# Kernel tuning notes

Measured on AMD Instinct MI355X. Metric: run time of the kernel, lower is better.

Reference implementation:

```python
import jax, jax.numpy as jnp
import numpy as np

N_HEAD, D_HEAD, D_MODEL = 16, 64, 1024
QLEN, MEMLEN, BSZ = 1024, 1024, 2
KLEN = QLEN + MEMLEN  # rlen == klen
LN_EPS = 1e-5
NEG = -1e30


def _rel_shift(x):
    # x: [qlen, rlen, bsz, n_head] -> Transformer-XL relative shift
    q, r, b, n = x.shape
    zp = jnp.zeros((q, 1, b, n), x.dtype)
    xp = jnp.concatenate([zp, x], axis=1).reshape(r + 1, q, b, n)
    return xp[1:].reshape(q, r, b, n)


def _layer_norm(x, gamma, beta):
    mu = jnp.mean(x, axis=-1, keepdims=True)
    var = jnp.mean((x - mu) ** 2, axis=-1, keepdims=True)
    return (x - mu) * jax.lax.rsqrt(var + LN_EPS) * gamma + beta


def setup_inputs() -> dict:
    key = jax.random.key(0)
    ks = jax.random.split(key, 8)
    w = jax.random.normal(ks[0], (QLEN, BSZ, D_MODEL), jnp.float32)
    r = jax.random.normal(ks[1], (KLEN, D_MODEL), jnp.float32)
    r_w_bias = jax.random.normal(ks[2], (N_HEAD, D_HEAD), jnp.float32) * 0.02
    r_r_bias = jax.random.normal(ks[3], (N_HEAD, D_HEAD), jnp.float32) * 0.02
    mems = jax.random.normal(ks[4], (MEMLEN, BSZ, D_MODEL), jnp.float32)
    W_qkv = jax.random.normal(ks[5], (D_MODEL, 3 * N_HEAD * D_HEAD), jnp.float32) * 0.02
    W_r = jax.random.normal(ks[6], (D_MODEL, N_HEAD * D_HEAD), jnp.float32) * 0.02
    W_o = jax.random.normal(ks[7], (N_HEAD * D_HEAD, D_MODEL), jnp.float32) * 0.02
    ln_gamma = jnp.ones((D_MODEL,), jnp.float32)
    ln_beta = jnp.zeros((D_MODEL,), jnp.float32)
    # causal mask with memory: key j visible to query i iff j <= i + MEMLEN (True = keep)
    attn_mask = jnp.arange(KLEN)[None, :] <= (jnp.arange(QLEN)[:, None] + MEMLEN)
    return {"w": w, "r": r, "r_w_bias": r_w_bias, "r_r_bias": r_r_bias,
            "mems": mems, "attn_mask": attn_mask, "W_qkv": W_qkv, "W_r": W_r,
            "W_o": W_o, "ln_gamma": ln_gamma, "ln_beta": ln_beta}


def reference(w, r, r_w_bias, r_r_bias, mems, attn_mask, W_qkv, W_r, W_o, ln_gamma, ln_beta):
    qlen, bsz = w.shape[0], w.shape[1]
    scale = 1.0 / (D_HEAD ** 0.5)
    cat = jnp.concatenate([mems, w], axis=0)            # [klen, b, d_model]
    klen = cat.shape[0]
    w_heads = cat @ W_qkv                                # [klen, b, 3*H*D]
    r_head_k = (r @ W_r).reshape(-1, N_HEAD, D_HEAD)     # [rlen, H, D]
    w_head_q, w_head_k, w_head_v = jnp.split(w_heads, 3, axis=-1)
    w_head_q = w_head_q[-qlen:].reshape(qlen, bsz, N_HEAD, D_HEAD)
    w_head_k = w_head_k.reshape(klen, bsz, N_HEAD, D_HEAD)
    w_head_v = w_head_v.reshape(klen, bsz, N_HEAD, D_HEAD)
    AC = jnp.einsum('ibnd,jbnd->ijbn', w_head_q + r_w_bias, w_head_k)
    BD = jnp.einsum('ibnd,jnd->ijbn', w_head_q + r_r_bias, r_head_k)
    BD = _rel_shift(BD)
    attn_score = (AC + BD) * scale                       # [q, k, b, n]
    attn_score = jnp.where(attn_mask[:, :, None, None], attn_score, NEG)
    attn_prob = jax.nn.softmax(attn_score, axis=1)
    attn_vec = jnp.einsum('ijbn,jbnd->ibnd', attn_prob, w_head_v)
    attn_vec = attn_vec.reshape(qlen, bsz, N_HEAD * D_HEAD)
    attn_out = attn_vec @ W_o                            # [q, b, d_model]
    return _layer_norm(w + attn_out, ln_gamma, ln_beta)
```

## Files before the change

kernel.cpp:

```cpp
#include <hip/hip_runtime.h>
#include <hip/hip_bf16.h>

#define NHEAD 16
#define DHEAD 64
#define DMODEL 1024
#define QLEN 1024
#define MEMLEN 1024
#define BSZ 2
#define KLEN 2048
#define LN_EPS 1e-5f

typedef __hip_bfloat16 bf16;
typedef __attribute__((ext_vector_type(8))) short short8;
typedef __attribute__((ext_vector_type(4))) float f32x4;

__device__ __forceinline__ float b2f(bf16 x) { return __bfloat162float(x); }
__device__ __forceinline__ bf16 f2b(float x) { return __float2bfloat16(x); }
__device__ __forceinline__ short f2bs(float f) {
    bf16 h = __float2bfloat16(f);
    return *reinterpret_cast<short*>(&h);
}
__device__ __forceinline__ float s2f(short s) {
    bf16 h = *reinterpret_cast<bf16*>(&s);
    return __bfloat162float(h);
}
__device__ __forceinline__ float fexp2(float x) {
    float y;
    asm("v_exp_f32 %0, %1" : "=v"(y) : "v"(x));
    return y;
}

#define MFMA16(a, b, c) __builtin_amdgcn_mfma_f32_16x16x32_bf16(a, b, c, 0, 0, 0)

#define AS1 __attribute__((address_space(1)))
#define AS3 __attribute__((address_space(3)))
__device__ __forceinline__ void gld16(const bf16* g, bf16* l) {
    __builtin_amdgcn_global_load_lds((const AS1 void*)(uintptr_t)g,
                                     (AS3 void*)(uint32_t)(uintptr_t)l, 16, 0, 0);
}

__global__ __launch_bounds__(256)
void prep(const float* __restrict__ mems, const float* __restrict__ w,
          const float* __restrict__ r, const float* __restrict__ Wqkv,
          const float* __restrict__ Wr, const float* __restrict__ Wo,
          bf16* __restrict__ Abf, bf16* __restrict__ rbf,
          bf16* __restrict__ Wqkvt, bf16* __restrict__ Wrt,
          bf16* __restrict__ Wot) {
    __shared__ bf16 T[64][65];
    const int id = blockIdx.x;
    const int t = threadIdx.x;
    if (id < 6144) {
        const float* src;
        bf16* dst;
        int off;
        if (id < 2048)      { src = mems; dst = Abf;                       off = id; }
        else if (id < 4096) { src = w;    dst = Abf + (size_t)2048 * 1024; off = id - 2048; }
        else                { src = r;    dst = rbf;                       off = id - 4096; }
        int i = off * 256 + t;
        const float4 v = reinterpret_cast<const float4*>(src)[i];
        bf16 o[4] = {f2b(v.x), f2b(v.y), f2b(v.z), f2b(v.w)};
        reinterpret_cast<ulong1*>(dst)[i] = *reinterpret_cast<ulong1*>(o);
        return;
    }
    int tid2 = id - 6144;
    const float* in;
    bf16* out;
    int N, tn, tile;
    if (tid2 < 768)       { in = Wqkv; out = Wqkvt; N = 3072; tn = 48; tile = tid2; }
    else if (tid2 < 1024) { in = Wr;   out = Wrt;   N = 1024; tn = 16; tile = tid2 - 768; }
    else                  { in = Wo;   out = Wot;   N = 1024; tn = 16; tile = tid2 - 1024; }
    const int K = 1024;
    const int n0 = (tile % tn) * 64, k0 = (tile / tn) * 64;
    #pragma unroll
    for (int e = 0; e < 16; e++) {
        int flat = e * 256 + t;
        int kl = flat >> 6, nl = flat & 63;
        T[kl][nl] = f2b(in[(size_t)(k0 + kl) * N + n0 + nl]);
    }
    __syncthreads();
    #pragma unroll
    for (int e = 0; e < 16; e++) {
        int flat = e * 256 + t;
        int nl = flat >> 6, kl = flat & 63;
        out[(size_t)(n0 + nl) * K + k0 + kl] = T[kl][nl];
    }
}

__global__ __launch_bounds__(256)
void gemm_mfma(const bf16* __restrict__ A, const bf16* __restrict__ Bt,
               const bf16* __restrict__ A2, const bf16* __restrict__ B2,
               int M, int N, int K, int mode,
               const float* __restrict__ rwb, const float* __restrict__ rrb,
               bf16* __restrict__ Qw, bf16* __restrict__ Qr,
               bf16* __restrict__ Kb, bf16* __restrict__ Vt,
               bf16* __restrict__ Cb, float* __restrict__ Cf,
               float* __restrict__ Cf2) {
    const int bm = blockIdx.x * 128, bn = blockIdx.y * 128;
    int sub = 0;
    const bf16* Ap = A;
    const bf16* Bp = Bt;
    if (mode == 0 && bm < 2048 && bn < 1024) { sub = 1; Ap = A2; Bp = B2; }
    const int ldk = (mode == 2) ? 1024 : K;
    float* Cfz = Cf;
    if (mode == 2 && blockIdx.z) { Ap += 512; Bp += 512; Cfz = Cf2; }
    __shared__ bf16 As[2][128 * 32];
    __shared__ bf16 Bs[2][128 * 32];
    const int t = threadIdx.x;
    const int w = t >> 6, lane = t & 63, quad = lane >> 4, l16 = lane & 15;
    const int wm = (w >> 1) * 64, wn = (w & 1) * 64;
    const int lrow = lane >> 2, lcol = (lane & 3) * 8;

    auto stage = [&](int k0, int buf) {
        #pragma unroll
        for (int e = 0; e < 2; e++) {
            int ch = w + 4 * e;
            int row = ch * 16 + lrow;
            gld16(Ap + (size_t)(bm + row) * ldk + k0 + lcol, As[buf] + ch * 512);
            gld16(Bp + (size_t)(bn + row) * ldk + k0 + lcol, Bs[buf] + ch * 512);
        }
    };

    f32x4 acc[4][4];
    #pragma unroll
    for (int mt = 0; mt < 4; mt++)
        #pragma unroll
        for (int nt = 0; nt < 4; nt++) acc[mt][nt] = (f32x4){0.f, 0.f, 0.f, 0.f};

    stage(0, 0);
    const int NK = K >> 5;
    for (int kk = 0; kk < NK; kk++) {
        asm volatile("s_waitcnt vmcnt(0)" ::: "memory");
        __builtin_amdgcn_s_barrier();
        if (kk + 1 < NK) stage((kk + 1) << 5, (kk + 1) & 1);
        const bf16* A_ = As[kk & 1];
        const bf16* B_ = Bs[kk & 1];
        short8 af[4], bfr[4];
        #pragma unroll
        for (int mt = 0; mt < 4; mt++)
            af[mt] = *reinterpret_cast<const short8*>(&A_[(wm + 16 * mt + l16) * 32 + quad * 8]);
        #pragma unroll
        for (int nt = 0; nt < 4; nt++)
            bfr[nt] = *reinterpret_cast<const short8*>(&B_[(wn + 16 * nt + l16) * 32 + quad * 8]);
        #pragma unroll
        for (int mt = 0; mt < 4; mt++)
            #pragma unroll
            for (int nt = 0; nt < 4; nt++)
                acc[mt][nt] = MFMA16(af[mt], bfr[nt], acc[mt][nt]);
    }

    const float QSC = 0.18033688f;
    #pragma unroll
    for (int mt = 0; mt < 4; mt++)
        #pragma unroll
        for (int nt = 0; nt < 4; nt++)
            #pragma unroll
            for (int r = 0; r < 4; r++) {
                int m = bm + wm + 16 * mt + quad * 4 + r;
                int c = bn + wn + 16 * nt + l16;
                float v = acc[mt][nt][r];
                if (sub) {
                    Cb[(size_t)m * 1024 + c] = f2b(v);
                } else if (mode == 0) {
                    int seg = c >> 10, cc2 = c & 1023;
                    if (seg == 0) {
                        if (m >= 2048) {
                            size_t o = (size_t)(m - 2048) * 1024 + cc2;
                            Qw[o] = f2b((v + rwb[cc2]) * QSC);
                            Qr[o] = f2b((v + rrb[cc2]) * QSC);
                        }
                    } else if (seg == 1) {
                        Kb[(size_t)m * 1024 + cc2] = f2b(v);
                    } else {
                        int j = m >> 1, bb = m & 1;
                        int vn = cc2 >> 6, dd = cc2 & 63;
                        int ds = dd >> 4, l16v = dd & 15;
                        int jt = j >> 6, jl = j & 63;
                        int h = jl >> 5, qd = (jl >> 3) & 3, e = jl & 7;
                        size_t addr = ((size_t)(vn * 2 + bb) * 32 + jt) * 4096
                                    + (ds * 2 + h) * 512 + (qd * 16 + l16v) * 8 + e;
                        Vt[addr] = f2b(v);
                    }
                } else {
                    Cfz[(size_t)m * N + c] = v;
                }
            }
}

__global__ __launch_bounds__(256, 3)
void attn_mfma(const bf16* __restrict__ Qw, const bf16* __restrict__ Qr,
               const bf16* __restrict__ Kb, const bf16* __restrict__ Vt,
               const bf16* __restrict__ Rk, float* __restrict__ O0g,
               float* __restrict__ O1g, float2* __restrict__ ML) {
    const int id = blockIdx.x;
    const int xcd = id & 7, local = id >> 3;
    const int pidx = local & 3;
    const int couple = (local >> 2) & 7;
    const int chunk = local >> 5;
    const int pair = xcd * 4 + pidx;
    const int b = pair & 1, n = pair >> 1;
    const int TA = couple + 17;
    const int t_beg = (chunk == 0) ? 0 : (chunk == 1) ? 17 : 33;
    const int t_end = (chunk == 0) ? 17 : (chunk == 1) ? 33 : 49;

    int segs[2][4];
    int nseg = 0;
    {
        int aend = min(t_end, TA);
        if (t_beg < aend) {
            segs[nseg][0] = couple; segs[nseg][1] = t_beg;
            segs[nseg][2] = aend;   segs[nseg][3] = (t_beg == 0) ? 0 : 1;
            nseg++;
        }
        int bbeg = max(t_beg, TA);
        if (bbeg < t_end) {
            segs[nseg][0] = 15 - couple; segs[nseg][1] = bbeg - TA;
            segs[nseg][2] = t_end - TA;  segs[nseg][3] = (bbeg == TA) ? 0 : 1;
            nseg++;
        }
    }

    const int tid = threadIdx.x;
    const int w = tid >> 6, lane = tid & 63;
    const int quad = lane >> 4, l16 = lane & 15;
    const int ln8 = lane >> 3;
    const int cs = (lane & 7) ^ (ln8 & 7);
    const int q0 = (quad ^ (l16 & 7)) * 8;
    const int q1 = q0 ^ 32;
    const int rbl = 48 - 16 * w;

    __shared__ bf16 Ks[64 * 64];
    __shared__ bf16 Vs[64 * 64];
    __shared__ bf16 Rs[3][64 * 64];
    __shared__ short WP_s[4][16 * 82];
    short* WP = WP_s[w];

    const int koff = b * 1024 + n * 64 + cs * 8;
    const bf16* Vbase = Vt + (size_t)(n * 2 + b) * 131072 + lane * 8;
    const int rcol = n * 64 + cs * 8;

    for (int sg = 0; sg < nseg; sg++) {
        const int i0 = segs[sg][0], jb = segs[sg][1], je = segs[sg][2], slot = segs[sg][3];
        const int I0 = i0 * 64;
        const int qbase = I0 + 16 * w;
        const int RB = 960 - I0;
        const int jlast = i0 + 16;

        auto stageKV = [&](int tt) {
            const int J0t = tt * 64;
            const bf16* vt = Vbase + (size_t)tt * 4096;
            #pragma unroll
            for (int e = 0; e < 2; e++) {
                int ch = w + 4 * e;
                gld16(vt + ch * 512, Vs + ch * 512);
                gld16(Kb + (size_t)(J0t + ch * 8 + ln8) * 2048 + koff, Ks + ch * 512);
            }
        };
        auto stageR = [&](int u) {
            bf16* rd = Rs[u % 3];
            #pragma unroll
            for (int e = 0; e < 2; e++) {
                int ch = w + 4 * e;
                int rrow = min(RB + u * 64 + ch * 8 + ln8, 2047);
                gld16(Rk + (size_t)rrow * 1024 + rcol, rd + ch * 512);
            }
        };

        short8 aqw[2], aqr[2];
        {
            const bf16* qp = Qw + ((size_t)(qbase + l16) * 2 + b) * 1024 + n * 64 + quad * 8;
            aqw[0] = *reinterpret_cast<const short8*>(qp);
            aqw[1] = *reinterpret_cast<const short8*>(qp + 32);
            const bf16* qp2 = Qr + ((size_t)(qbase + l16) * 2 + b) * 1024 + n * 64 + quad * 8;
            aqr[0] = *reinterpret_cast<const short8*>(qp2);
            aqr[1] = *reinterpret_cast<const short8*>(qp2 + 32);
        }

        f32x4 O[4];
        #pragma unroll
        for (int d = 0; d < 4; d++) O[d] = (f32x4){0.f, 0.f, 0.f, 0.f};
        float m_run = -1e30f;
        float pl[4] = {0.f, 0.f, 0.f, 0.f};

        if (sg) {
            asm volatile("s_waitcnt vmcnt(0)" ::: "memory");
            __builtin_amdgcn_s_barrier();
        }
        stageR(jb); stageR(jb + 1);

        for (int j = jb; j < je; j++) {
            const int J0 = j * 64;

            asm volatile("s_waitcnt vmcnt(0)" ::: "memory");
            __builtin_amdgcn_s_barrier();

            stageKV(j);
            stageR(j + 2);

            const bf16* R0 = Rs[j % 3];
            const bf16* R1 = Rs[(j + 1) % 3];

            #pragma unroll
            for (int s = 0; s < 5; s++) {
                int rb2 = rbl + 16 * s;
                const bf16* Rb = (rb2 & 64) ? R1 : R0;
                int rh = (rb2 & 63) + l16;
                short8 b0 = *reinterpret_cast<const short8*>(&Rb[rh * 64 + q0]);
                short8 b1 = *reinterpret_cast<const short8*>(&Rb[rh * 64 + q1]);
                f32x4 acc = (f32x4){0.f, 0.f, 0.f, 0.f};
                __builtin_amdgcn_s_setprio(1);
                acc = MFMA16(aqr[0], b0, acc);
                acc = MFMA16(aqr[1], b1, acc);
                __builtin_amdgcn_s_setprio(0);
                #pragma unroll
                for (int r = 0; r < 4; r++)
                    WP[(quad * 4 + r) * 82 + 16 * s + l16] = f2bs(acc[r]);
            }

            asm volatile("s_waitcnt vmcnt(2)" ::: "memory");
            __builtin_amdgcn_s_barrier();

            float sv[4][4];
            #pragma unroll
            for (int n16 = 0; n16 < 4; n16++) {
                int kr = 16 * n16 + l16;
                short8 k0 = *reinterpret_cast<const short8*>(&Ks[kr * 64 + q0]);
                short8 k1 = *reinterpret_cast<const short8*>(&Ks[kr * 64 + q1]);
                f32x4 acc = (f32x4){0.f, 0.f, 0.f, 0.f};
                __builtin_amdgcn_s_setprio(1);
                acc = MFMA16(aqw[0], k0, acc);
                acc = MFMA16(aqw[1], k1, acc);
                __builtin_amdgcn_s_setprio(0);
                #pragma unroll
                for (int r = 0; r < 4; r++) {
                    int row = quad * 4 + r, col = 16 * n16 + l16;
                    sv[n16][r] = acc[r] + s2f(WP[row * 82 + col - row + 15]);
                }
            }
            if (j == jlast) {
                #pragma unroll
                for (int n16 = 0; n16 < 4; n16++)
                    #pragma unroll
                    for (int r = 0; r < 4; r++) {
                        int row = quad * 4 + r, col = 16 * n16 + l16;
                        if (J0 + col > qbase + row + MEMLEN) sv[n16][r] = -1e30f;
                    }
            }

            float mx = sv[0][0];
            #pragma unroll
            for (int n16 = 0; n16 < 4; n16++)
                #pragma unroll
                for (int r = 0; r < 4; r++) mx = fmaxf(mx, sv[n16][r]);
            #pragma unroll
            for (int msk = 1; msk < 16; msk <<= 1) mx = fmaxf(mx, __shfl_xor(mx, msk));
            if (mx > m_run + 11.5f) {
                const float alpha = fexp2(m_run - mx);
                m_run = mx;
                #pragma unroll
                for (int r = 0; r < 4; r++) pl[r] *= alpha;
                #pragma unroll
                for (int d = 0; d < 4; d++)
                    #pragma unroll
                    for (int r = 0; r < 4; r++) O[d][r] *= alpha;
            }
            #pragma unroll
            for (int n16 = 0; n16 < 4; n16++)
                #pragma unroll
                for (int r = 0; r < 4; r++) sv[n16][r] = fexp2(sv[n16][r] - m_run);
            #pragma unroll
            for (int r = 0; r < 4; r++)
                pl[r] += sv[0][r] + sv[1][r] + sv[2][r] + sv[3][r];

            #pragma unroll
            for (int n16 = 0; n16 < 4; n16++)
                #pragma unroll
                for (int r = 0; r < 4; r++)
                    WP[(quad * 4 + r) * 72 + 16 * n16 + l16] = f2bs(sv[n16][r]);
            short8 ap0 = *reinterpret_cast<short8*>(&WP[l16 * 72 + quad * 8]);
            short8 ap1 = *reinterpret_cast<short8*>(&WP[l16 * 72 + 32 + quad * 8]);

            __builtin_amdgcn_s_setprio(1);
            #pragma unroll
            for (int ds = 0; ds < 4; ds++) {
                short8 v0 = *reinterpret_cast<const short8*>(&Vs[(ds * 2 + 0) * 512 + lane * 8]);
                short8 v1 = *reinterpret_cast<const short8*>(&Vs[(ds * 2 + 1) * 512 + lane * 8]);
                O[ds] = MFMA16(ap0, v0, O[ds]);
                O[ds] = MFMA16(ap1, v1, O[ds]);
            }
            __builtin_amdgcn_s_setprio(0);
        }

        float lr[4];
        #pragma unroll
        for (int r = 0; r < 4; r++) {
            float s = pl[r];
            #pragma unroll
            for (int msk = 1; msk < 16; msk <<= 1) s += __shfl_xor(s, msk);
            lr[r] = s;
        }
        if (l16 == 0) {
            #pragma unroll
            for (int r = 0; r < 4; r++) {
                int q = qbase + quad * 4 + r;
                ML[(size_t)slot * 32768 + (q * 2 + b) * 16 + n] =
                    make_float2(m_run, lr[r]);
            }
        }
        float* Od = slot ? O1g : O0g;
        #pragma unroll
        for (int ds = 0; ds < 4; ds++)
            #pragma unroll
            for (int r = 0; r < 4; r++) {
                int q = qbase + quad * 4 + r;
                Od[((size_t)q * 2 + b) * 1024 + n * 64 + 16 * ds + l16] = O[ds][r];
            }
    }
}

__global__ __launch_bounds__(256)
void attn_combine(const float* __restrict__ O0, const float* __restrict__ O1,
                  const float2* __restrict__ ML, bf16* __restrict__ AVbf) {
    const int row = blockIdx.x;
    const int t = threadIdx.x;
    const int n = t >> 4;
    const int i0 = row >> 7;
    const float2 a0 = ML[row * 16 + n];
    const f32x4 p0 = reinterpret_cast<const f32x4*>(O0)[row * 256 + t];
    short o[4];
    if (i0 != 0) {
        const float2 a1 = ML[32768 + row * 16 + n];
        const float m = fmaxf(a0.x, a1.x);
        const float e0 = fexp2(a0.x - m);
        const float e1 = fexp2(a1.x - m);
        const float inv = 1.f / (a0.y * e0 + a1.y * e1);
        const f32x4 p1 = reinterpret_cast<const f32x4*>(O1)[row * 256 + t];
        #pragma unroll
        for (int jj = 0; jj < 4; jj++)
            o[jj] = f2bs((p0[jj] * e0 + p1[jj] * e1) * inv);
    } else {
        const float inv = 1.f / a0.y;
        #pragma unroll
        for (int jj = 0; jj < 4; jj++) o[jj] = f2bs(p0[jj] * inv);
    }
    reinterpret_cast<ulong1*>(AVbf)[row * 256 + t] = *reinterpret_cast<ulong1*>(o);
}

__global__ __launch_bounds__(256)
void ln_res(const float* __restrict__ ao0, const float* __restrict__ ao1,
            const float* __restrict__ w, const float* __restrict__ gamma,
            const float* __restrict__ beta, float* __restrict__ out) {
    const int m = blockIdx.x;
    const int t = threadIdx.x;
    const int wv = t >> 6, lane = t & 63;
    __shared__ float red[8];
    float x[4];
    #pragma unroll
    for (int e = 0; e < 4; e++) {
        int c = e * 256 + t;
        x[e] = ao0[(size_t)m * DMODEL + c] + ao1[(size_t)m * DMODEL + c]
             + w[(size_t)m * DMODEL + c];
    }
    float s = x[0] + x[1] + x[2] + x[3];
    #pragma unroll
    for (int msk = 1; msk < 64; msk <<= 1) s += __shfl_xor(s, msk);
    if (lane == 0) red[wv] = s;
    __syncthreads();
    const float mu = (red[0] + red[1] + red[2] + red[3]) * (1.f / 1024.f);
    float s2 = 0.f;
    #pragma unroll
    for (int e = 0; e < 4; e++) { float dx = x[e] - mu; s2 += dx * dx; }
    #pragma unroll
    for (int msk = 1; msk < 64; msk <<= 1) s2 += __shfl_xor(s2, msk);
    if (lane == 0) red[4 + wv] = s2;
    __syncthreads();
    const float rstd = rsqrtf((red[4] + red[5] + red[6] + red[7]) * (1.f / 1024.f) + LN_EPS);
    #pragma unroll
    for (int e = 0; e < 4; e++) {
        int c = e * 256 + t;
        out[(size_t)m * DMODEL + c] = (x[e] - mu) * rstd * gamma[c] + beta[c];
    }
}

extern "C" void kernel_launch(void* const* d_in, const int* in_sizes, int n_in,
                              void* d_out, int out_size, void* d_ws, size_t ws_size,
                              hipStream_t stream) {
    const float* w        = (const float*)d_in[0];
    const float* r        = (const float*)d_in[1];
    const float* r_w_bias = (const float*)d_in[2];
    const float* r_r_bias = (const float*)d_in[3];
    const float* mems     = (const float*)d_in[4];
    const float* W_qkv    = (const float*)d_in[6];
    const float* W_r      = (const float*)d_in[7];
    const float* W_o      = (const float*)d_in[8];
    const float* gamma    = (const float*)d_in[9];
    const float* beta     = (const float*)d_in[10];
    float* out = (float*)d_out;

    bf16* Abf    = (bf16*)d_ws;
    bf16* Wqkvt  = Abf   + (size_t)4096 * 1024;
    bf16* Wrt    = Wqkvt + (size_t)3072 * 1024;
    bf16* Wot    = Wrt   + (size_t)1024 * 1024;
    bf16* rbf    = Wot   + (size_t)1024 * 1024;
    bf16* Qw     = rbf   + (size_t)2048 * 1024;
    bf16* Qr     = Qw    + (size_t)2048 * 1024;
    bf16* Kb     = Qr    + (size_t)2048 * 1024;
    bf16* Vt     = Kb    + (size_t)4096 * 1024;
    bf16* Rk     = Vt    + (size_t)2048 * 2048;
    bf16* AVbf   = Rk    + (size_t)2048 * 1024;
    float* Opart0   = (float*)Abf;
    float* Opart1   = (float*)Wqkvt;
    float2* ML      = (float2*)rbf;
    float* attn_out0 = (float*)Abf;
    float* attn_out1 = (float*)Wqkvt;

    dim3 b256(256);
    prep<<<dim3(7424), b256, 0, stream>>>(mems, w, r, W_qkv, W_r, W_o,
                                          Abf, rbf, Wqkvt, Wrt, Wot);
    gemm_mfma<<<dim3(32, 24), b256, 0, stream>>>(
        Abf, Wqkvt, rbf, Wrt, 4096, 3072, 1024, 0, r_w_bias, r_r_bias,
        Qw, Qr, Kb, Vt, Rk, nullptr, nullptr);
    attn_mfma<<<dim3(768), b256, 0, stream>>>(Qw, Qr, Kb, Vt, Rk,
                                              Opart0, Opart1, ML);
    attn_combine<<<dim3(2048), b256, 0, stream>>>(Opart0, Opart1, ML, AVbf);
    gemm_mfma<<<dim3(16, 8, 2), b256, 0, stream>>>(
        AVbf, Wot, nullptr, nullptr, 2048, 1024, 512, 2, nullptr, nullptr,
        nullptr, nullptr, nullptr, nullptr, nullptr, attn_out0, attn_out1);
    ln_res<<<dim3(QLEN * BSZ), b256, 0, stream>>>(attn_out0, attn_out1, w,
                                                  gamma, beta, out);
}
```

Measured before the change: 242.2 us.

## Split attention into four chunks, load V directly to registers, shrink LDS

The attention work split goes from 3 to 4 chunks per head pair (grid 768 to 1024), and a third partial-output buffer is added for rows whose work spans three chunks. The combine kernel now merges up to three partial softmax states. V fragments are loaded straight from global memory into registers instead of being staged through LDS. The R buffer drops from triple to double buffering, with its prefetch moved after the barrier. Together these are meant to raise occupancy and parallelism and cut LDS traffic, at the cost of more partial outputs to merge and V loads exposed on the critical path. The ML buffer now lives in the output buffer, relying on ln_res overwriting it later.

```diff
diff --git a/kernel.cpp b/kernel.cpp
--- a/kernel.cpp
+++ b/kernel.cpp
@@ -190,7 +190,8 @@
 void attn_mfma(const bf16* __restrict__ Qw, const bf16* __restrict__ Qr,
                const bf16* __restrict__ Kb, const bf16* __restrict__ Vt,
                const bf16* __restrict__ Rk, float* __restrict__ O0g,
-               float* __restrict__ O1g, float2* __restrict__ ML) {
+               float* __restrict__ O1g, float* __restrict__ O2g,
+               float2* __restrict__ ML) {
     const int id = blockIdx.x;
     const int xcd = id & 7, local = id >> 3;
     const int pidx = local & 3;
@@ -199,22 +200,22 @@
     const int pair = xcd * 4 + pidx;
     const int b = pair & 1, n = pair >> 1;
     const int TA = couple + 17;
-    const int t_beg = (chunk == 0) ? 0 : (chunk == 1) ? 17 : 33;
-    const int t_end = (chunk == 0) ? 17 : (chunk == 1) ? 33 : 49;
+    const int t0 = (chunk == 0) ? 0 : (chunk == 1) ? 13 : (chunk == 2) ? 25 : 37;
+    const int t1 = (chunk == 0) ? 13 : (chunk == 1) ? 25 : (chunk == 2) ? 37 : 49;
 
     int segs[2][4];
     int nseg = 0;
     {
-        int aend = min(t_end, TA);
-        if (t_beg < aend) {
-            segs[nseg][0] = couple; segs[nseg][1] = t_beg;
-            segs[nseg][2] = aend;   segs[nseg][3] = (t_beg == 0) ? 0 : 1;
+        int aend = min(t1, TA);
+        if (t0 < aend) {
+            segs[nseg][0] = couple; segs[nseg][1] = t0;
+            segs[nseg][2] = aend;   segs[nseg][3] = (chunk == 0) ? 0 : 1;
             nseg++;
         }
-        int bbeg = max(t_beg, TA);
-        if (bbeg < t_end) {
+        int bbeg = max(t0, TA);
+        if (bbeg < t1) {
             segs[nseg][0] = 15 - couple; segs[nseg][1] = bbeg - TA;
-            segs[nseg][2] = t_end - TA;  segs[nseg][3] = (bbeg == TA) ? 0 : 1;
+            segs[nseg][2] = t1 - TA;     segs[nseg][3] = chunk - 1;
             nseg++;
         }
     }
@@ -229,8 +230,7 @@
     const int rbl = 48 - 16 * w;
 
     __shared__ bf16 Ks[64 * 64];
-    __shared__ bf16 Vs[64 * 64];
-    __shared__ bf16 Rs[3][64 * 64];
+    __shared__ bf16 Rs[2][64 * 64];
     __shared__ short WP_s[4][16 * 82];
     short* WP = WP_s[w];
 
@@ -245,18 +245,16 @@
         const int RB = 960 - I0;
         const int jlast = i0 + 16;
 
-        auto stageKV = [&](int tt) {
+        auto stageK = [&](int tt) {
             const int J0t = tt * 64;
-            const bf16* vt = Vbase + (size_t)tt * 4096;
             #pragma unroll
             for (int e = 0; e < 2; e++) {
                 int ch = w + 4 * e;
-                gld16(vt + ch * 512, Vs + ch * 512);
                 gld16(Kb + (size_t)(J0t + ch * 8 + ln8) * 2048 + koff, Ks + ch * 512);
             }
         };
         auto stageR = [&](int u) {
-            bf16* rd = Rs[u % 3];
+            bf16* rd = Rs[u & 1];
             #pragma unroll
             for (int e = 0; e < 2; e++) {
                 int ch = w + 4 * e;
@@ -293,11 +291,21 @@
             asm volatile("s_waitcnt vmcnt(0)" ::: "memory");
             __builtin_amdgcn_s_barrier();
 
-            stageKV(j);
-            stageR(j + 2);
-
-            const bf16* R0 = Rs[j % 3];
-            const bf16* R1 = Rs[(j + 1) % 3];
+            stageK(j);
+            __builtin_amdgcn_sched_barrier(0);
+            short8 vf0[4], vf1[4];
+            {
+                const bf16* vp = Vbase + (size_t)j * 4096;
+                #pragma unroll
+                for (int ds = 0; ds < 4; ds++) {
+                    vf0[ds] = *reinterpret_cast<const short8*>(vp + (ds * 2 + 0) * 512);
+                    vf1[ds] = *reinterpret_cast<const short8*>(vp + (ds * 2 + 1) * 512);
+                }
+            }
+            __builtin_amdgcn_sched_barrier(0);
+
+            const bf16* R0 = Rs[j & 1];
+            const bf16* R1 = Rs[(j + 1) & 1];
 
             #pragma unroll
             for (int s = 0; s < 5; s++) {
@@ -316,8 +324,10 @@
                     WP[(quad * 4 + r) * 82 + 16 * s + l16] = f2bs(acc[r]);
             }
 
-            asm volatile("s_waitcnt vmcnt(2)" ::: "memory");
+            asm volatile("s_waitcnt vmcnt(8)" ::: "memory");
             __builtin_amdgcn_s_barrier();
+
+            if (j + 2 <= je) stageR(j + 2);
 
             float sv[4][4];
             #pragma unroll
@@ -382,10 +392,8 @@
             __builtin_amdgcn_s_setprio(1);
             #pragma unroll
             for (int ds = 0; ds < 4; ds++) {
-                short8 v0 = *reinterpret_cast<const short8*>(&Vs[(ds * 2 + 0) * 512 + lane * 8]);
-                short8 v1 = *reinterpret_cast<const short8*>(&Vs[(ds * 2 + 1) * 512 + lane * 8]);
-                O[ds] = MFMA16(ap0, v0, O[ds]);
-                O[ds] = MFMA16(ap1, v1, O[ds]);
+                O[ds] = MFMA16(ap0, vf0[ds], O[ds]);
+                O[ds] = MFMA16(ap1, vf1[ds], O[ds]);
             }
             __builtin_amdgcn_s_setprio(0);
         }
@@ -406,42 +414,46 @@
                     make_float2(m_run, lr[r]);
             }
         }
-        float* Od = slot ? O1g : O0g;
+        float* Od = (slot == 0) ? O0g : (slot == 1) ? O1g : O2g;
+        const int roff = (slot == 2) ? 1024 : 0;
         #pragma unroll
         for (int ds = 0; ds < 4; ds++)
             #pragma unroll
             for (int r = 0; r < 4; r++) {
                 int q = qbase + quad * 4 + r;
-                Od[((size_t)q * 2 + b) * 1024 + n * 64 + 16 * ds + l16] = O[ds][r];
+                Od[((size_t)(q * 2 + b - roff)) * 1024 + n * 64 + 16 * ds + l16] = O[ds][r];
             }
     }
 }
 
 __global__ __launch_bounds__(256)
 void attn_combine(const float* __restrict__ O0, const float* __restrict__ O1,
-                  const float2* __restrict__ ML, bf16* __restrict__ AVbf) {
+                  const float* __restrict__ O2, const float2* __restrict__ ML,
+                  bf16* __restrict__ AVbf) {
     const int row = blockIdx.x;
     const int t = threadIdx.x;
     const int n = t >> 4;
     const int i0 = row >> 7;
     const float2 a0 = ML[row * 16 + n];
+    const float2 a1 = ML[32768 + row * 16 + n];
     const f32x4 p0 = reinterpret_cast<const f32x4*>(O0)[row * 256 + t];
+    const f32x4 p1 = reinterpret_cast<const f32x4*>(O1)[row * 256 + t];
+    float m = fmaxf(a0.x, a1.x);
+    float2 a2 = make_float2(0.f, 0.f);
+    f32x4 p2 = (f32x4){0.f, 0.f, 0.f, 0.f};
+    if (i0 >= 8) {
+        a2 = ML[65536 + row * 16 + n];
+        m = fmaxf(m, a2.x);
+        p2 = reinterpret_cast<const f32x4*>(O2)[(row - 1024) * 256 + t];
+    }
+    const float e0 = fexp2(a0.x - m);
+    const float e1 = fexp2(a1.x - m);
+    const float e2 = (i0 >= 8) ? fexp2(a2.x - m) : 0.f;
+    const float inv = 1.f / (a0.y * e0 + a1.y * e1 + a2.y * e2);
     short o[4];
-    if (i0 != 0) {
-        const float2 a1 = ML[32768 + row * 16 + n];
-        const float m = fmaxf(a0.x, a1.x);
-        const float e0 = fexp2(a0.x - m);
-        const float e1 = fexp2(a1.x - m);
-        const float inv = 1.f / (a0.y * e0 + a1.y * e1);
-        const f32x4 p1 = reinterpret_cast<const f32x4*>(O1)[row * 256 + t];
-        #pragma unroll
-        for (int jj = 0; jj < 4; jj++)
-            o[jj] = f2bs((p0[jj] * e0 + p1[jj] * e1) * inv);
-    } else {
-        const float inv = 1.f / a0.y;
-        #pragma unroll
-        for (int jj = 0; jj < 4; jj++) o[jj] = f2bs(p0[jj] * inv);
-    }
+    #pragma unroll
+    for (int jj = 0; jj < 4; jj++)
+        o[jj] = f2bs((p0[jj] * e0 + p1[jj] * e1 + p2[jj] * e2) * inv);
     reinterpret_cast<ulong1*>(AVbf)[row * 256 + t] = *reinterpret_cast<ulong1*>(o);
 }
 
@@ -509,7 +521,8 @@
     bf16* AVbf   = Rk    + (size_t)2048 * 1024;
     float* Opart0   = (float*)Abf;
     float* Opart1   = (float*)Wqkvt;
-    float2* ML      = (float2*)rbf;
+    float* Opart2   = (float*)rbf;
+    float2* ML      = (float2*)out;
     float* attn_out0 = (float*)Abf;
     float* attn_out1 = (float*)Wqkvt;
 
@@ -519,9 +532,9 @@
     gemm_mfma<<<dim3(32, 24), b256, 0, stream>>>(
         Abf, Wqkvt, rbf, Wrt, 4096, 3072, 1024, 0, r_w_bias, r_r_bias,
         Qw, Qr, Kb, Vt, Rk, nullptr, nullptr);
-    attn_mfma<<<dim3(768), b256, 0, stream>>>(Qw, Qr, Kb, Vt, Rk,
-                                              Opart0, Opart1, ML);
-    attn_combine<<<dim3(2048), b256, 0, stream>>>(Opart0, Opart1, ML, AVbf);
+    attn_mfma<<<dim3(1024), b256, 0, stream>>>(Qw, Qr, Kb, Vt, Rk,
+                                               Opart0, Opart1, Opart2, ML);
+    attn_combine<<<dim3(2048), b256, 0, stream>>>(Opart0, Opart1, Opart2, ML, AVbf);
     gemm_mfma<<<dim3(16, 8, 2), b256, 0, stream>>>(
         AVbf, Wot, nullptr, nullptr, 2048, 1024, 512, 2, nullptr, nullptr,
         nullptr, nullptr, nullptr, nullptr, nullptr, attn_out0, attn_out1);
```

Result: no change. 244.1 us (+0.8%).

## Fuse attention combine into Wo GEMM and triple-buffer QKV GEMM loads

Applied to the files above, without the earlier changes.

Removes the separate attn_combine kernel. The Wo GEMM now reads the fp32 partial outputs and softmax stats, merges them, and converts them to bf16 while staging its A tile, so the intermediate AV buffer and one launch are dropped. The QKV GEMM is specialised and moves to a three-stage LDS pipeline with a partial vmcnt wait so loads can overlap compute. The Wo GEMM also gets an XCD-aware block mapping. The cost is more LDS per block in the QKV GEMM, and redundant combine arithmetic in Wo, since each A tile is recomputed by all 8 N-blocks.

```diff
diff --git a/kernel.cpp b/kernel.cpp
--- a/kernel.cpp
+++ b/kernel.cpp
@@ -87,24 +87,19 @@
 }
 
 __global__ __launch_bounds__(256)
-void gemm_mfma(const bf16* __restrict__ A, const bf16* __restrict__ Bt,
-               const bf16* __restrict__ A2, const bf16* __restrict__ B2,
-               int M, int N, int K, int mode,
-               const float* __restrict__ rwb, const float* __restrict__ rrb,
-               bf16* __restrict__ Qw, bf16* __restrict__ Qr,
-               bf16* __restrict__ Kb, bf16* __restrict__ Vt,
-               bf16* __restrict__ Cb, float* __restrict__ Cf,
-               float* __restrict__ Cf2) {
+void gemm_qkv(const bf16* __restrict__ A, const bf16* __restrict__ Bt,
+              const bf16* __restrict__ A2, const bf16* __restrict__ B2,
+              const float* __restrict__ rwb, const float* __restrict__ rrb,
+              bf16* __restrict__ Qw, bf16* __restrict__ Qr,
+              bf16* __restrict__ Kb, bf16* __restrict__ Vt,
+              bf16* __restrict__ Cb) {
     const int bm = blockIdx.x * 128, bn = blockIdx.y * 128;
     int sub = 0;
     const bf16* Ap = A;
     const bf16* Bp = Bt;
-    if (mode == 0 && bm < 2048 && bn < 1024) { sub = 1; Ap = A2; Bp = B2; }
-    const int ldk = (mode == 2) ? 1024 : K;
-    float* Cfz = Cf;
-    if (mode == 2 && blockIdx.z) { Ap += 512; Bp += 512; Cfz = Cf2; }
-    __shared__ bf16 As[2][128 * 32];
-    __shared__ bf16 Bs[2][128 * 32];
+    if (bm < 2048 && bn < 1024) { sub = 1; Ap = A2; Bp = B2; }
+    __shared__ bf16 As[3][128 * 32];
+    __shared__ bf16 Bs[3][128 * 32];
     const int t = threadIdx.x;
     const int w = t >> 6, lane = t & 63, quad = lane >> 4, l16 = lane & 15;
     const int wm = (w >> 1) * 64, wn = (w & 1) * 64;
@@ -115,8 +110,8 @@
         for (int e = 0; e < 2; e++) {
             int ch = w + 4 * e;
             int row = ch * 16 + lrow;
-            gld16(Ap + (size_t)(bm + row) * ldk + k0 + lcol, As[buf] + ch * 512);
-            gld16(Bp + (size_t)(bn + row) * ldk + k0 + lcol, Bs[buf] + ch * 512);
+            gld16(Ap + (size_t)(bm + row) * 1024 + k0 + lcol, As[buf] + ch * 512);
+            gld16(Bp + (size_t)(bn + row) * 1024 + k0 + lcol, Bs[buf] + ch * 512);
         }
     };
 
@@ -127,13 +122,15 @@
         for (int nt = 0; nt < 4; nt++) acc[mt][nt] = (f32x4){0.f, 0.f, 0.f, 0.f};
 
     stage(0, 0);
-    const int NK = K >> 5;
+    stage(32, 1);
+    const int NK = 32;
     for (int kk = 0; kk < NK; kk++) {
-        asm volatile("s_waitcnt vmcnt(0)" ::: "memory");
+        if (kk + 1 < NK) asm volatile("s_waitcnt vmcnt(4)" ::: "memory");
+        else             asm volatile("s_waitcnt vmcnt(0)" ::: "memory");
         __builtin_amdgcn_s_barrier();
-        if (kk + 1 < NK) stage((kk + 1) << 5, (kk + 1) & 1);
-        const bf16* A_ = As[kk & 1];
-        const bf16* B_ = Bs[kk & 1];
+        if (kk + 2 < NK) stage((kk + 2) << 5, (kk + 2) % 3);
+        const bf16* A_ = As[kk % 3];
+        const bf16* B_ = Bs[kk % 3];
         short8 af[4], bfr[4];
         #pragma unroll
         for (int mt = 0; mt < 4; mt++)
@@ -160,7 +157,7 @@
                 float v = acc[mt][nt][r];
                 if (sub) {
                     Cb[(size_t)m * 1024 + c] = f2b(v);
-                } else if (mode == 0) {
+                } else {
                     int seg = c >> 10, cc2 = c & 1023;
                     if (seg == 0) {
                         if (m >= 2048) {
@@ -180,8 +177,6 @@
                                     + (ds * 2 + h) * 512 + (qd * 16 + l16v) * 8 + e;
                         Vt[addr] = f2b(v);
                     }
-                } else {
-                    Cfz[(size_t)m * N + c] = v;
                 }
             }
 }
@@ -418,31 +413,97 @@
 }
 
 __global__ __launch_bounds__(256)
-void attn_combine(const float* __restrict__ O0, const float* __restrict__ O1,
-                  const float2* __restrict__ ML, bf16* __restrict__ AVbf) {
-    const int row = blockIdx.x;
+void wo_gemm(const float* __restrict__ O0, const float* __restrict__ O1,
+             const float2* __restrict__ ML, const bf16* __restrict__ Wot,
+             float* __restrict__ C0, float* __restrict__ C1) {
+    const int lid = blockIdx.x;
+    const int xcd = lid & 7, q = lid >> 3;
+    const int bmi = xcd * 2 + (q & 1);
+    const int bni = (q >> 1) & 7;
+    const int z = q >> 4;
+    const int bm = bmi * 128, bn = bni * 128, kz = z * 512;
+    float* Cfz = z ? C1 : C0;
+    const bool two = (bmi != 0);
+
+    __shared__ bf16 As[2][128 * 32];
+    __shared__ bf16 Bs[2][128 * 32];
     const int t = threadIdx.x;
-    const int n = t >> 4;
-    const int i0 = row >> 7;
-    const float2 a0 = ML[row * 16 + n];
-    const f32x4 p0 = reinterpret_cast<const f32x4*>(O0)[row * 256 + t];
-    short o[4];
-    if (i0 != 0) {
-        const float2 a1 = ML[32768 + row * 16 + n];
+    const int w = t >> 6, lane = t & 63, quad = lane >> 4, l16 = lane & 15;
+    const int wm = (w >> 1) * 64, wn = (w & 1) * 64;
+    const int lrow = lane >> 2, lcol = (lane & 3) * 8;
+    const int arow = t >> 1, acl = (t & 1) * 16;
+    const int grow = bm + arow;
+
+    auto stageA = [&](int k0, int buf) {
+        const int c = kz + k0 + acl;
+        const int n = c >> 6;
+        const float2 a0 = ML[grow * 16 + n];
+        const float2 a1 = two ? ML[32768 + grow * 16 + n] : make_float2(-3e38f, 0.f);
         const float m = fmaxf(a0.x, a1.x);
         const float e0 = fexp2(a0.x - m);
         const float e1 = fexp2(a1.x - m);
         const float inv = 1.f / (a0.y * e0 + a1.y * e1);
-        const f32x4 p1 = reinterpret_cast<const f32x4*>(O1)[row * 256 + t];
-        #pragma unroll
-        for (int jj = 0; jj < 4; jj++)
-            o[jj] = f2bs((p0[jj] * e0 + p1[jj] * e1) * inv);
-    } else {
-        const float inv = 1.f / a0.y;
-        #pragma unroll
-        for (int jj = 0; jj < 4; jj++) o[jj] = f2bs(p0[jj] * inv);
-    }
-    reinterpret_cast<ulong1*>(AVbf)[row * 256 + t] = *reinterpret_cast<ulong1*>(o);
+        const f32x4* p0 = reinterpret_cast<const f32x4*>(&O0[(size_t)grow * 1024 + c]);
+        const f32x4* p1 = reinterpret_cast<const f32x4*>(&O1[(size_t)grow * 1024 + c]);
+        short o[16];
+        #pragma unroll
+        for (int u = 0; u < 4; u++) {
+            f32x4 v0 = p0[u];
+            f32x4 v1 = two ? p1[u] : (f32x4){0.f, 0.f, 0.f, 0.f};
+            #pragma unroll
+            for (int jj = 0; jj < 4; jj++)
+                o[u * 4 + jj] = f2bs((v0[jj] * e0 + v1[jj] * e1) * inv);
+        }
+        *reinterpret_cast<short8*>(&As[buf][arow * 32 + acl])     = *reinterpret_cast<short8*>(o);
+        *reinterpret_cast<short8*>(&As[buf][arow * 32 + acl + 8]) = *reinterpret_cast<short8*>(o + 8);
+    };
+    auto stageB = [&](int k0, int buf) {
+        #pragma unroll
+        for (int e = 0; e < 2; e++) {
+            int ch = w + 4 * e;
+            int row = ch * 16 + lrow;
+            gld16(Wot + (size_t)(bn + row) * 1024 + kz + k0 + lcol, Bs[buf] + ch * 512);
+        }
+    };
+
+    f32x4 acc[4][4];
+    #pragma unroll
+    for (int mt = 0; mt < 4; mt++)
+        #pragma unroll
+        for (int nt = 0; nt < 4; nt++) acc[mt][nt] = (f32x4){0.f, 0.f, 0.f, 0.f};
+
+    stageB(0, 0);
+    stageA(0, 0);
+    const int NK = 16;
+    for (int kk = 0; kk < NK; kk++) {
+        __syncthreads();
+        if (kk + 1 < NK) { stageB((kk + 1) << 5, (kk + 1) & 1); stageA((kk + 1) << 5, (kk + 1) & 1); }
+        const bf16* A_ = As[kk & 1];
+        const bf16* B_ = Bs[kk & 1];
+        short8 af[4], bfr[4];
+        #pragma unroll
+        for (int mt = 0; mt < 4; mt++)
+            af[mt] = *reinterpret_cast<const short8*>(&A_[(wm + 16 * mt + l16) * 32 + quad * 8]);
+        #pragma unroll
+        for (int nt = 0; nt < 4; nt++)
+            bfr[nt] = *reinterpret_cast<const short8*>(&B_[(wn + 16 * nt + l16) * 32 + quad * 8]);
+        #pragma unroll
+        for (int mt = 0; mt < 4; mt++)
+            #pragma unroll
+            for (int nt = 0; nt < 4; nt++)
+                acc[mt][nt] = MFMA16(af[mt], bfr[nt], acc[mt][nt]);
+    }
+
+    #pragma unroll
+    for (int mt = 0; mt < 4; mt++)
+        #pragma unroll
+        for (int nt = 0; nt < 4; nt++)
+            #pragma unroll
+            for (int r = 0; r < 4; r++) {
+                int m = bm + wm + 16 * mt + quad * 4 + r;
+                int c = bn + wn + 16 * nt + l16;
+                Cfz[(size_t)m * 1024 + c] = acc[mt][nt][r];
+            }
 }
 
 __global__ __launch_bounds__(256)
@@ -506,25 +567,21 @@
     bf16* Kb     = Qr    + (size_t)2048 * 1024;
     bf16* Vt     = Kb    + (size_t)4096 * 1024;
     bf16* Rk     = Vt    + (size_t)2048 * 2048;
-    bf16* AVbf   = Rk    + (size_t)2048 * 1024;
     float* Opart0   = (float*)Abf;
     float* Opart1   = (float*)Wqkvt;
     float2* ML      = (float2*)rbf;
-    float* attn_out0 = (float*)Abf;
-    float* attn_out1 = (float*)Wqkvt;
+    float* attn_out0 = (float*)Kb;
+    float* attn_out1 = (float*)Vt;
 
     dim3 b256(256);
     prep<<<dim3(7424), b256, 0, stream>>>(mems, w, r, W_qkv, W_r, W_o,
                                           Abf, rbf, Wqkvt, Wrt, Wot);
-    gemm_mfma<<<dim3(32, 24), b256, 0, stream>>>(
-        Abf, Wqkvt, rbf, Wrt, 4096, 3072, 1024, 0, r_w_bias, r_r_bias,
-        Qw, Qr, Kb, Vt, Rk, nullptr, nullptr);
+    gemm_qkv<<<dim3(32, 24), b256, 0, stream>>>(
+        Abf, Wqkvt, rbf, Wrt, r_w_bias, r_r_bias, Qw, Qr, Kb, Vt, Rk);
     attn_mfma<<<dim3(768), b256, 0, stream>>>(Qw, Qr, Kb, Vt, Rk,
                                               Opart0, Opart1, ML);
-    attn_combine<<<dim3(2048), b256, 0, stream>>>(Opart0, Opart1, ML, AVbf);
-    gemm_mfma<<<dim3(16, 8, 2), b256, 0, stream>>>(
-        AVbf, Wot, nullptr, nullptr, 2048, 1024, 512, 2, nullptr, nullptr,
-        nullptr, nullptr, nullptr, nullptr, nullptr, attn_out0, attn_out1);
+    wo_gemm<<<dim3(256), b256, 0, stream>>>(Opart0, Opart1, ML, Wot,
+                                            attn_out0, attn_out1);
     ln_res<<<dim3(QLEN * BSZ), b256, 0, stream>>>(attn_out0, attn_out1, w,
                                                   gamma, beta, out);
 }
```

New measurement: 239.0 us. Within noise of the previous version (-1.4%).
